# Performance work log

Measured on AMD Instinct MI355X. Metric: run time of the kernel, lower is better.

The kernel has to match this reference:

```python
import jax, jax.numpy as jnp
import numpy as np

HEADS = 8
DIM_HEAD = 96
INNER = HEADS * DIM_HEAD  # 768
PEP_DIM = 768
PRO_DIM = 768
SCALE = DIM_HEAD ** -0.5
NEG = -1000000.0
EPS = 1e-5


def _layer_norm(x, g, b):
    mu = jnp.mean(x, axis=-1, keepdims=True)
    var = jnp.mean(jnp.square(x - mu), axis=-1, keepdims=True)
    return (x - mu) * jax.lax.rsqrt(var + EPS) * g + b


def setup_inputs() -> dict:
    key = jax.random.key(0)
    ks = jax.random.split(key, 12)
    b, n, m = 16, 128, 2048
    peptide = jax.random.normal(ks[0], (b, n, PEP_DIM), dtype=jnp.float32)
    protein = jax.random.normal(ks[1], (b, m, PRO_DIM), dtype=jnp.float32)
    peptide_mask = jax.random.randint(ks[2], (b, n), 0, 2, dtype=jnp.int32)
    pro_mask = jax.random.randint(ks[3], (b, m), 0, 2, dtype=jnp.int32)
    s = 0.02
    Wq = jax.random.normal(ks[4], (PEP_DIM, INNER), dtype=jnp.float32) * s
    Wk = jax.random.normal(ks[5], (PRO_DIM, INNER), dtype=jnp.float32) * s
    Wv_prot = jax.random.normal(ks[6], (PRO_DIM, INNER), dtype=jnp.float32) * s
    Wv_pep = jax.random.normal(ks[7], (PEP_DIM, INNER), dtype=jnp.float32) * s
    Wo_prot = jax.random.normal(ks[8], (INNER, PEP_DIM), dtype=jnp.float32) * s
    bo_prot = jnp.zeros((PEP_DIM,), dtype=jnp.float32)
    Wo_pep = jax.random.normal(ks[9], (INNER, PRO_DIM), dtype=jnp.float32) * s
    bo_pep = jnp.zeros((PRO_DIM,), dtype=jnp.float32)
    ln_g = jnp.ones((PEP_DIM,), dtype=jnp.float32)
    ln_b = jnp.zeros((PEP_DIM,), dtype=jnp.float32)
    return {
        'peptide': peptide, 'protein': protein,
        'peptide_mask': peptide_mask, 'pro_mask': pro_mask,
        'Wq': Wq, 'Wk': Wk, 'Wv_prot': Wv_prot, 'Wv_pep': Wv_pep,
        'Wo_prot': Wo_prot, 'bo_prot': bo_prot,
        'Wo_pep': Wo_pep, 'bo_pep': bo_pep,
        'ln_g': ln_g, 'ln_b': ln_b,
    }


def reference(peptide, protein, peptide_mask, pro_mask,
              Wq, Wk, Wv_prot, Wv_pep, Wo_prot, bo_prot, Wo_pep, bo_pep,
              ln_g, ln_b):
    b, n, _ = peptide.shape
    m = protein.shape[1]
    # projections -> (b, h, len, d)
    q = (peptide @ Wq).reshape(b, n, HEADS, DIM_HEAD).transpose(0, 2, 1, 3)
    k = (protein @ Wk).reshape(b, m, HEADS, DIM_HEAD).transpose(0, 2, 1, 3)
    v_prot = (protein @ Wv_prot).reshape(b, m, HEADS, DIM_HEAD).transpose(0, 2, 1, 3)
    v_pep = (peptide @ Wv_pep).reshape(b, n, HEADS, DIM_HEAD).transpose(0, 2, 1, 3)
    # scores (b, h, n, m)
    dots = jnp.einsum('bhnd,bhmd->bhnm', q, k) * SCALE
    dots = jnp.where(peptide_mask[:, None, :, None] == 0, NEG, dots)
    dots = jnp.where(pro_mask[:, None, None, :] == 0, NEG, dots)
    attn = jax.nn.softmax(dots, axis=-1)
    # peptide-side output: rows of attn aggregate protein values
    out_protein = jnp.einsum('bhnm,bhmd->bhnd', attn, v_prot)
    out_protein = out_protein.transpose(0, 2, 1, 3).reshape(b, n, INNER)
    out_protein = out_protein @ Wo_prot + bo_prot
    out_protein = _layer_norm(out_protein + peptide, ln_g, ln_b)
    # protein-side output: attn^T aggregates peptide values
    out_peptide = jnp.einsum('bhnm,bhnd->bhmd', attn, v_pep)
    out_peptide = out_peptide.transpose(0, 2, 1, 3).reshape(b, m, INNER)
    out_peptide = out_peptide @ Wo_pep + bo_pep
    out_peptide = _layer_norm(out_peptide + protein, ln_g, ln_b)
    return (out_protein, out_peptide, attn)
```

## Files before the change

### kernel.cpp

```cpp
#include <hip/hip_runtime.h>
#include <math.h>

static constexpr int HEADS  = 8;
static constexpr int DHEAD  = 96;
static constexpr int INNER  = 768;
static constexpr int NPEP   = 128;
static constexpr int MPRO   = 2048;
static constexpr float ATT_SCALE = 0.10206207261596577f;
static constexpr float NEGF   = -1000000.0f;
static constexpr float LN_EPS = 1e-5f;

typedef __attribute__((ext_vector_type(8))) short bf16x8;
typedef __attribute__((ext_vector_type(4))) float f32x4;

__device__ __forceinline__ unsigned short f2b(float f) {
    unsigned u = __builtin_bit_cast(unsigned, f);
    u += 0x7fffu + ((u >> 16) & 1u);
    return (unsigned short)(u >> 16);
}
__device__ __forceinline__ float b2f(unsigned short u) {
    return __builtin_bit_cast(float, (unsigned)u << 16);
}

__device__ __forceinline__ void async16(const unsigned short* g, unsigned short* l) {
    __builtin_amdgcn_global_load_lds(
        (const __attribute__((address_space(1))) void*)g,
        (__attribute__((address_space(3))) void*)l, 16, 0, 0);
}

template<int TM, int MODE>
__global__ __launch_bounds__(256) void gemm_bf16(
    const unsigned short* __restrict__ A, const unsigned short* __restrict__ B,
    unsigned short* __restrict__ C,
    int M, int N, int K, int lda, int ldb, int ldc,
    long sAb, long sAh, long sBb, long sBh, long sCb, long sCh,
    const int* __restrict__ mRow, const int* __restrict__ mCol, int lenShift)
{
    constexpr int FR = TM / 32;
    __shared__ unsigned short As[TM * 32];
    __shared__ unsigned short Bs[128 * 32];

    const int tid = threadIdx.x;
    const int n0  = blockIdx.x * 128;
    const int m0  = blockIdx.y * TM;
    const int z   = blockIdx.z;
    const int zb  = z >> 3, zh = z & 7;

    const unsigned short* Ab = A + zb * sAb + zh * sAh;
    const unsigned short* Bb = B + zb * sBb + zh * sBh;

    const int rS = tid >> 2;
    const int kS = (tid & 3) * 8;
    const int wave = tid >> 6;
    unsigned short* ldsA0 = As + wave * 512;
    unsigned short* ldsA1 = As + 2048 + wave * 512;
    unsigned short* ldsB0 = Bs + wave * 512;
    unsigned short* ldsB1 = Bs + 2048 + wave * 512;

    const int lane = tid & 63;
    const int l16  = lane & 15;
    const int quad = lane >> 4;
    const int wr   = (wave >> 1) * (TM / 2);
    const int wc   = (wave & 1) * 64;

    f32x4 acc[FR][4];
#pragma unroll
    for (int i = 0; i < FR; ++i)
#pragma unroll
        for (int j = 0; j < 4; ++j) acc[i][j] = (f32x4){0.f, 0.f, 0.f, 0.f};

    for (int k0 = 0; k0 < K; k0 += 32) {
        async16(Ab + (long)(m0 + rS) * lda + k0 + kS, ldsA0);
        if (TM == 128)
            async16(Ab + (long)(m0 + 64 + rS) * lda + k0 + kS, ldsA1);
        int bR0 = n0 + rS;      if (bR0 > N - 1) bR0 = N - 1;
        int bR1 = n0 + 64 + rS; if (bR1 > N - 1) bR1 = N - 1;
        async16(Bb + (long)bR0 * ldb + k0 + kS, ldsB0);
        async16(Bb + (long)bR1 * ldb + k0 + kS, ldsB1);
        __syncthreads();

        bf16x8 af[FR], bfr[4];
#pragma unroll
        for (int i = 0; i < FR; ++i)
            af[i] = *reinterpret_cast<const bf16x8*>(&As[(wr + i * 16 + l16) * 32 + quad * 8]);
#pragma unroll
        for (int j = 0; j < 4; ++j)
            bfr[j] = *reinterpret_cast<const bf16x8*>(&Bs[(wc + j * 16 + l16) * 32 + quad * 8]);
#pragma unroll
        for (int i = 0; i < FR; ++i)
#pragma unroll
            for (int j = 0; j < 4; ++j)
                acc[i][j] = __builtin_amdgcn_mfma_f32_16x16x32_bf16(af[i], bfr[j], acc[i][j], 0, 0, 0);
        __syncthreads();
    }

#pragma unroll
    for (int i = 0; i < FR; ++i) {
#pragma unroll
        for (int j = 0; j < 4; ++j) {
            const int col = n0 + wc + j * 16 + l16;
            if ((MODE == 2) && col >= N) continue;
            const int h = col / 96, d = col - h * 96;
#pragma unroll
            for (int r = 0; r < 4; ++r) {
                const int row = m0 + wr + i * 16 + quad * 4 + r;
                float v = acc[i][j][r];
                if (MODE == 1) {
                    v *= ATT_SCALE;
                    if (mRow[zb * NPEP + row] == 0 || mCol[zb * MPRO + col] == 0) v = NEGF;
                    C[zb * sCb + zh * sCh + (long)row * ldc + col] = f2b(v);
                } else if (MODE == 2) {
                    C[zb * sCb + zh * sCh + (long)row * ldc + col] = f2b(v);
                } else if (MODE == 3) {
                    const int b = row >> lenShift, rr = row & ((1 << lenShift) - 1);
                    C[(((long)(b * 8 + h) << lenShift) + rr) * 96 + d] = f2b(v);
                } else {
                    const int b = row >> lenShift, rr = row & ((1 << lenShift) - 1);
                    C[(((long)(b * 8 + h) * 96 + d) << lenShift) + rr] = f2b(v);
                }
            }
        }
    }
}

__global__ __launch_bounds__(256) void pv2_kernel(
    const unsigned short* __restrict__ attn16,
    const unsigned short* __restrict__ vpepT,
    unsigned short* __restrict__ opep)
{
    __shared__ unsigned short At[128 * 136];
    __shared__ unsigned short Bv[128 * 136];

    const int tid = threadIdx.x;
    const int m0  = blockIdx.x * 128;
    const int z   = blockIdx.y;
    const int b   = z >> 3, h = z & 7;

    const unsigned short* Az = attn16 + (long)z * NPEP * MPRO;
    const unsigned short* Bz = vpepT + (long)z * 96 * 128;

    {
        const int r = tid >> 1, half = tid & 1;
        const int rc = r > 95 ? 95 : r;
#pragma unroll
        for (int e = 0; e < 8; ++e) {
            bf16x8 v = *reinterpret_cast<const bf16x8*>(Bz + rc * 128 + half * 64 + e * 8);
            *reinterpret_cast<bf16x8*>(&Bv[r * 136 + half * 64 + e * 8]) = v;
        }
    }
    {
        const int mBase = (tid & 7) * 16;
#pragma unroll
        for (int nn = 0; nn < 128; nn += 32) {
            const int n = nn + (tid >> 3);
#pragma unroll
            for (int c = 0; c < 2; ++c) {
                bf16x8 v = *reinterpret_cast<const bf16x8*>(Az + (long)n * MPRO + m0 + mBase + c * 8);
#pragma unroll
                for (int j = 0; j < 8; ++j)
                    At[(mBase + c * 8 + j) * 136 + n] = (unsigned short)v[j];
            }
        }
    }
    __syncthreads();

    const int lane = tid & 63;
    const int l16  = lane & 15;
    const int quad = lane >> 4;
    const int wave = tid >> 6;
    const int wr   = (wave >> 1) * 64;
    const int wc   = (wave & 1) * 64;

    f32x4 acc[4][4];
#pragma unroll
    for (int i = 0; i < 4; ++i)
#pragma unroll
        for (int j = 0; j < 4; ++j) acc[i][j] = (f32x4){0.f, 0.f, 0.f, 0.f};

#pragma unroll
    for (int kc = 0; kc < 4; ++kc) {
        bf16x8 af[4], bfr[4];
#pragma unroll
        for (int i = 0; i < 4; ++i)
            af[i] = *reinterpret_cast<const bf16x8*>(&At[(wr + i * 16 + l16) * 136 + kc * 32 + quad * 8]);
#pragma unroll
        for (int j = 0; j < 4; ++j)
            bfr[j] = *reinterpret_cast<const bf16x8*>(&Bv[(wc + j * 16 + l16) * 136 + kc * 32 + quad * 8]);
#pragma unroll
        for (int i = 0; i < 4; ++i)
#pragma unroll
            for (int j = 0; j < 4; ++j)
                acc[i][j] = __builtin_amdgcn_mfma_f32_16x16x32_bf16(af[i], bfr[j], acc[i][j], 0, 0, 0);
    }

#pragma unroll
    for (int i = 0; i < 4; ++i) {
#pragma unroll
        for (int j = 0; j < 4; ++j) {
            const int d = wc + j * 16 + l16;
            if (d >= 96) continue;
#pragma unroll
            for (int r = 0; r < 4; ++r) {
                const int m = m0 + wr + i * 16 + quad * 4 + r;
                opep[(long)b * MPRO * INNER + (long)m * INNER + h * 96 + d] = f2b(acc[i][j][r]);
            }
        }
    }
}

__global__ __launch_bounds__(256) void conv2_kernel(
    const float* __restrict__ pro, const float* __restrict__ pep,
    unsigned short* __restrict__ pro16, unsigned short* __restrict__ pep16,
    int nPro4, int nPep4)
{
    const int i = blockIdx.x * 256 + threadIdx.x;
    const float* in; unsigned short* out; int idx;
    if (i < nPro4) { in = pro; out = pro16; idx = i; }
    else { idx = i - nPro4; if (idx >= nPep4) return; in = pep; out = pep16; }
    float4 v = reinterpret_cast<const float4*>(in)[idx];
    ushort4 o;
    o.x = f2b(v.x); o.y = f2b(v.y); o.z = f2b(v.z); o.w = f2b(v.w);
    reinterpret_cast<ushort4*>(out)[idx] = o;
}

__global__ __launch_bounds__(256) void wtrans_kernel(
    const float* w0, const float* w1, const float* w2,
    const float* w3, const float* w4, const float* w5,
    unsigned short* o0, unsigned short* o1, unsigned short* o2,
    unsigned short* o3, unsigned short* o4, unsigned short* o5)
{
    const float* in; unsigned short* out;
    switch (blockIdx.z) {
        case 0: in = w0; out = o0; break;
        case 1: in = w1; out = o1; break;
        case 2: in = w2; out = o2; break;
        case 3: in = w3; out = o3; break;
        case 4: in = w4; out = o4; break;
        default: in = w5; out = o5; break;
    }
    __shared__ unsigned short t[32][33];
    const int bx = blockIdx.x * 32, by = blockIdx.y * 32;
    const int x = threadIdx.x, y = threadIdx.y;
#pragma unroll
    for (int i = 0; i < 32; i += 8)
        t[y + i][x] = f2b(in[(long)(by + y + i) * 768 + bx + x]);
    __syncthreads();
#pragma unroll
    for (int i = 0; i < 32; i += 8)
        out[(long)(bx + y + i) * 768 + by + x] = t[x][y + i];
}

__global__ __launch_bounds__(256) void softmax_kernel(
    unsigned short* __restrict__ s16, float* __restrict__ attn)
{
    __shared__ float smx[4], sms[4];
    const long row = blockIdx.x;
    unsigned short* p16 = s16 + row * (long)MPRO;
    float* pf = attn + row * (long)MPRO;
    const int tid = threadIdx.x;
    const int wv = tid >> 6;

    float v[8];
    float mx = -3.4e38f;
#pragma unroll
    for (int k = 0; k < 8; ++k) { v[k] = b2f(p16[tid + k * 256]); mx = fmaxf(mx, v[k]); }
#pragma unroll
    for (int off = 32; off > 0; off >>= 1) mx = fmaxf(mx, __shfl_xor(mx, off));
    if ((tid & 63) == 0) smx[wv] = mx;
    __syncthreads();
    mx = fmaxf(fmaxf(smx[0], smx[1]), fmaxf(smx[2], smx[3]));

    float sum = 0.f;
#pragma unroll
    for (int k = 0; k < 8; ++k) { v[k] = __expf(v[k] - mx); sum += v[k]; }
#pragma unroll
    for (int off = 32; off > 0; off >>= 1) sum += __shfl_xor(sum, off);
    if ((tid & 63) == 0) sms[wv] = sum;
    __syncthreads();
    const float inv = 1.0f / (sms[0] + sms[1] + sms[2] + sms[3]);
#pragma unroll
    for (int k = 0; k < 8; ++k) {
        const float o = v[k] * inv;
        pf[tid + k * 256] = o;
        p16[tid + k * 256] = f2b(o);
    }
}

__global__ __launch_bounds__(256) void bias_res_ln(
    const unsigned short* __restrict__ tmp, const float* __restrict__ bias,
    const float* __restrict__ res, const float* __restrict__ gam,
    const float* __restrict__ bet, float* __restrict__ out)
{
    __shared__ float red[8];
    const long row = blockIdx.x;
    const unsigned short* t = tmp + row * INNER;
    const float* r = res + row * INNER;
    float* o = out + row * INNER;
    const int tid = threadIdx.x;
    const int wv = tid >> 6;

    float v[3]; float s = 0.f;
#pragma unroll
    for (int k = 0; k < 3; ++k) { const int c = tid + k * 256; v[k] = b2f(t[c]) + bias[c] + r[c]; s += v[k]; }
#pragma unroll
    for (int off = 32; off > 0; off >>= 1) s += __shfl_xor(s, off);
    if ((tid & 63) == 0) red[wv] = s;
    __syncthreads();
    const float mu = (red[0] + red[1] + red[2] + red[3]) * (1.0f / INNER);

    float vs = 0.f;
#pragma unroll
    for (int k = 0; k < 3; ++k) { const float d = v[k] - mu; vs += d * d; }
#pragma unroll
    for (int off = 32; off > 0; off >>= 1) vs += __shfl_xor(vs, off);
    if ((tid & 63) == 0) red[4 + wv] = vs;
    __syncthreads();
    const float rstd = rsqrtf((red[4] + red[5] + red[6] + red[7]) * (1.0f / INNER) + LN_EPS);
#pragma unroll
    for (int k = 0; k < 3; ++k) { const int c = tid + k * 256; o[c] = (v[k] - mu) * rstd * gam[c] + bet[c]; }
}

extern "C" void kernel_launch(void* const* d_in, const int* in_sizes, int n_in,
                              void* d_out, int out_size, void* d_ws, size_t ws_size,
                              hipStream_t stream)
{
    (void)in_sizes; (void)n_in; (void)out_size; (void)ws_size;

    const float* peptide = (const float*)d_in[0];
    const float* protein = (const float*)d_in[1];
    const int*   pepm    = (const int*)  d_in[2];
    const int*   prom    = (const int*)  d_in[3];
    const float* Wq      = (const float*)d_in[4];
    const float* Wk      = (const float*)d_in[5];
    const float* Wv_prot = (const float*)d_in[6];
    const float* Wv_pep  = (const float*)d_in[7];
    const float* Wo_prot = (const float*)d_in[8];
    const float* bo_prot = (const float*)d_in[9];
    const float* Wo_pep  = (const float*)d_in[10];
    const float* bo_pep  = (const float*)d_in[11];
    const float* ln_g    = (const float*)d_in[12];
    const float* ln_b    = (const float*)d_in[13];

    char* ws = (char*)d_ws;
    auto U = [&](size_t off) { return (unsigned short*)(ws + off); };
    unsigned short* WT0   = U(0);
    unsigned short* WT1   = U(1179648);
    unsigned short* WT2   = U(2 * 1179648);
    unsigned short* WT3   = U(3 * 1179648);
    unsigned short* WT4   = U(4 * 1179648);
    unsigned short* WT5   = U(5 * 1179648);
    unsigned short* q16   = U(7077888);
    unsigned short* k16   = U(10223616);
    unsigned short* vpT   = U(60555264);
    unsigned short* vpepT = U(110886912);
    unsigned short* s16   = U(114032640);
    unsigned short* pro16 = U(114032640);
    unsigned short* pep16 = U(164364288);
    unsigned short* opp   = U(7077888);
    unsigned short* tmp1  = U(10223616);
    unsigned short* opep  = U(13369344);
    unsigned short* tmp2  = U(63700992);

    float* outP = (float*)d_out;
    float* outQ = outP + 16 * 128 * 768;
    float* attn = outQ + (long)16 * 2048 * 768;

    conv2_kernel<<<26112, 256, 0, stream>>>(protein, peptide, pro16, pep16, 6291456, 393216);
    wtrans_kernel<<<dim3(24, 24, 6), dim3(32, 8), 0, stream>>>(
        Wq, Wk, Wv_prot, Wv_pep, Wo_prot, Wo_pep, WT0, WT1, WT2, WT3, WT4, WT5);

    gemm_bf16<128, 3><<<dim3(6, 16, 1), 256, 0, stream>>>(
        pep16, WT0, q16, 2048, 768, 768, 768, 768, 0,
        0, 0, 0, 0, 0, 0, nullptr, nullptr, 7);
    gemm_bf16<128, 3><<<dim3(6, 256, 1), 256, 0, stream>>>(
        pro16, WT1, k16, 32768, 768, 768, 768, 768, 0,
        0, 0, 0, 0, 0, 0, nullptr, nullptr, 11);
    gemm_bf16<128, 4><<<dim3(6, 256, 1), 256, 0, stream>>>(
        pro16, WT2, vpT, 32768, 768, 768, 768, 768, 0,
        0, 0, 0, 0, 0, 0, nullptr, nullptr, 11);
    gemm_bf16<128, 4><<<dim3(6, 16, 1), 256, 0, stream>>>(
        pep16, WT3, vpepT, 2048, 768, 768, 768, 768, 0,
        0, 0, 0, 0, 0, 0, nullptr, nullptr, 7);

    gemm_bf16<128, 1><<<dim3(16, 1, 128), 256, 0, stream>>>(
        q16, k16, s16, 128, 2048, 96, 96, 96, 2048,
        98304L, 12288L, 1572864L, 196608L, 2097152L, 262144L, pepm, prom, 0);

    softmax_kernel<<<16384, 256, 0, stream>>>(s16, attn);

    gemm_bf16<64, 2><<<dim3(1, 2, 128), 256, 0, stream>>>(
        s16, vpT, opp, 128, 96, 2048, 2048, 2048, 768,
        2097152L, 262144L, 1572864L, 196608L, 98304L, 96L, nullptr, nullptr, 0);

    gemm_bf16<64, 2><<<dim3(6, 32, 1), 256, 0, stream>>>(
        opp, WT4, tmp1, 2048, 768, 768, 768, 768, 768,
        0, 0, 0, 0, 0, 0, nullptr, nullptr, 0);
    bias_res_ln<<<2048, 256, 0, stream>>>(tmp1, bo_prot, peptide, ln_g, ln_b, outP);

    pv2_kernel<<<dim3(16, 128), 256, 0, stream>>>(s16, vpepT, opep);

    gemm_bf16<128, 2><<<dim3(6, 256, 1), 256, 0, stream>>>(
        opep, WT5, tmp2, 32768, 768, 768, 768, 768, 768,
        0, 0, 0, 0, 0, 0, nullptr, nullptr, 0);
    bias_res_ln<<<32768, 256, 0, stream>>>(tmp2, bo_pep, protein, ln_g, ln_b, outQ);
}
```

Before: 831.3 us.

## Triple-buffer GEMM LDS loads, swizzle large-GEMM blocks, move masking into softmax

The bf16 GEMM now keeps three LDS stages of async global-to-LDS loads in flight. It waits on explicit vmcnt counts and raw barriers instead of a sync per k-step, and raises wave priority around the MFMA block. The large protein-side GEMMs use a flattened 1D grid with an XCD-aware block swizzle to improve L2 locality. Score masking moves out of the QK GEMM epilogue into the softmax kernel, which reads the peptide and protein masks itself. The extra LDS stages use more shared memory and may lower occupancy, and the hand-written waitcnt values depend on the exact number of async loads issued per stage.

```diff
diff --git a/kernel.cpp b/kernel.cpp
--- a/kernel.cpp
+++ b/kernel.cpp
@@ -34,15 +34,25 @@
     unsigned short* __restrict__ C,
     int M, int N, int K, int lda, int ldb, int ldc,
     long sAb, long sAh, long sBb, long sBh, long sCb, long sCh,
-    const int* __restrict__ mRow, const int* __restrict__ mCol, int lenShift)
-{
-    constexpr int FR = TM / 32;
-    __shared__ unsigned short As[TM * 32];
-    __shared__ unsigned short Bs[128 * 32];
+    const int* __restrict__ mRow, const int* __restrict__ mCol, int lenShift,
+    int nxSwz)
+{
+    (void)mRow; (void)mCol; (void)M;
+    constexpr int FR   = TM / 32;
+    constexpr int PIPE = 3;
+    __shared__ unsigned short As[PIPE][TM * 32];
+    __shared__ unsigned short Bs[PIPE][128 * 32];
 
     const int tid = threadIdx.x;
-    const int n0  = blockIdx.x * 128;
-    const int m0  = blockIdx.y * TM;
+    int bx, by;
+    if (nxSwz > 0) {
+        const int bid = blockIdx.x;
+        const int per = gridDim.x >> 3;
+        const int v   = (bid & 7) * per + (bid >> 3);
+        bx = v % nxSwz; by = v / nxSwz;
+    } else { bx = blockIdx.x; by = blockIdx.y; }
+    const int n0  = bx * 128;
+    const int m0  = by * TM;
     const int z   = blockIdx.z;
     const int zb  = z >> 3, zh = z & 7;
 
@@ -52,10 +62,6 @@
     const int rS = tid >> 2;
     const int kS = (tid & 3) * 8;
     const int wave = tid >> 6;
-    unsigned short* ldsA0 = As + wave * 512;
-    unsigned short* ldsA1 = As + 2048 + wave * 512;
-    unsigned short* ldsB0 = Bs + wave * 512;
-    unsigned short* ldsB1 = Bs + 2048 + wave * 512;
 
     const int lane = tid & 63;
     const int l16  = lane & 15;
@@ -69,29 +75,58 @@
 #pragma unroll
         for (int j = 0; j < 4; ++j) acc[i][j] = (f32x4){0.f, 0.f, 0.f, 0.f};
 
-    for (int k0 = 0; k0 < K; k0 += 32) {
-        async16(Ab + (long)(m0 + rS) * lda + k0 + kS, ldsA0);
+    auto stageT = [&](int t, int bi) {
+        const int k0 = t << 5;
+        unsigned short* a0 = &As[bi][wave * 512];
+        async16(Ab + (long)(m0 + rS) * lda + k0 + kS, a0);
         if (TM == 128)
-            async16(Ab + (long)(m0 + 64 + rS) * lda + k0 + kS, ldsA1);
+            async16(Ab + (long)(m0 + 64 + rS) * lda + k0 + kS, a0 + 2048);
         int bR0 = n0 + rS;      if (bR0 > N - 1) bR0 = N - 1;
         int bR1 = n0 + 64 + rS; if (bR1 > N - 1) bR1 = N - 1;
-        async16(Bb + (long)bR0 * ldb + k0 + kS, ldsB0);
-        async16(Bb + (long)bR1 * ldb + k0 + kS, ldsB1);
-        __syncthreads();
+        unsigned short* b0 = &Bs[bi][wave * 512];
+        async16(Bb + (long)bR0 * ldb + k0 + kS, b0);
+        async16(Bb + (long)bR1 * ldb + k0 + kS, b0 + 2048);
+    };
+
+    const int NT = K >> 5;
+    stageT(0, 0);
+    if (NT > 1) stageT(1, 1);
+    if (NT > 2) stageT(2, 2);
+
+    int bi = 0;
+    for (int t = 0; t < NT; ++t) {
+        const int ahead = NT - 1 - t;
+        if constexpr (TM == 128) {
+            if (ahead >= 2)      asm volatile("s_waitcnt vmcnt(8)" ::: "memory");
+            else if (ahead == 1) asm volatile("s_waitcnt vmcnt(4)" ::: "memory");
+            else                 asm volatile("s_waitcnt vmcnt(0)" ::: "memory");
+        } else {
+            if (ahead >= 2)      asm volatile("s_waitcnt vmcnt(6)" ::: "memory");
+            else if (ahead == 1) asm volatile("s_waitcnt vmcnt(3)" ::: "memory");
+            else                 asm volatile("s_waitcnt vmcnt(0)" ::: "memory");
+        }
+        __builtin_amdgcn_s_barrier();
 
         bf16x8 af[FR], bfr[4];
 #pragma unroll
         for (int i = 0; i < FR; ++i)
-            af[i] = *reinterpret_cast<const bf16x8*>(&As[(wr + i * 16 + l16) * 32 + quad * 8]);
+            af[i] = *reinterpret_cast<const bf16x8*>(&As[bi][(wr + i * 16 + l16) * 32 + quad * 8]);
 #pragma unroll
         for (int j = 0; j < 4; ++j)
-            bfr[j] = *reinterpret_cast<const bf16x8*>(&Bs[(wc + j * 16 + l16) * 32 + quad * 8]);
+            bfr[j] = *reinterpret_cast<const bf16x8*>(&Bs[bi][(wc + j * 16 + l16) * 32 + quad * 8]);
+
+        __builtin_amdgcn_s_setprio(1);
 #pragma unroll
         for (int i = 0; i < FR; ++i)
 #pragma unroll
             for (int j = 0; j < 4; ++j)
                 acc[i][j] = __builtin_amdgcn_mfma_f32_16x16x32_bf16(af[i], bfr[j], acc[i][j], 0, 0, 0);
-        __syncthreads();
+        __builtin_amdgcn_s_setprio(0);
+
+        __builtin_amdgcn_s_barrier();
+        __builtin_amdgcn_sched_barrier(0);
+        if (t + PIPE < NT) stageT(t + PIPE, bi);
+        bi = bi + 1; if (bi == PIPE) bi = 0;
     }
 
 #pragma unroll
@@ -107,7 +142,6 @@
                 float v = acc[i][j][r];
                 if (MODE == 1) {
                     v *= ATT_SCALE;
-                    if (mRow[zb * NPEP + row] == 0 || mCol[zb * MPRO + col] == 0) v = NEGF;
                     C[zb * sCb + zh * sCh + (long)row * ldc + col] = f2b(v);
                 } else if (MODE == 2) {
                     C[zb * sCb + zh * sCh + (long)row * ldc + col] = f2b(v);
@@ -251,19 +285,34 @@
 }
 
 __global__ __launch_bounds__(256) void softmax_kernel(
-    unsigned short* __restrict__ s16, float* __restrict__ attn)
+    unsigned short* __restrict__ s16, float* __restrict__ attn,
+    const int* __restrict__ pepm, const int* __restrict__ prom)
 {
     __shared__ float smx[4], sms[4];
     const long row = blockIdx.x;
+    const int b = (int)(row >> 10);
+    const int n = (int)(row & 127);
     unsigned short* p16 = s16 + row * (long)MPRO;
     float* pf = attn + row * (long)MPRO;
     const int tid = threadIdx.x;
     const int wv = tid >> 6;
+    const int rowOk = pepm[(b << 7) + n];
 
     float v[8];
     float mx = -3.4e38f;
-#pragma unroll
-    for (int k = 0; k < 8; ++k) { v[k] = b2f(p16[tid + k * 256]); mx = fmaxf(mx, v[k]); }
+    if (rowOk) {
+#pragma unroll
+        for (int k = 0; k < 8; ++k) {
+            const int c = tid + k * 256;
+            float x = b2f(p16[c]);
+            if (prom[(b << 11) + c] == 0) x = NEGF;
+            v[k] = x; mx = fmaxf(mx, x);
+        }
+    } else {
+#pragma unroll
+        for (int k = 0; k < 8; ++k) v[k] = NEGF;
+        mx = NEGF;
+    }
 #pragma unroll
     for (int off = 32; off > 0; off >>= 1) mx = fmaxf(mx, __shfl_xor(mx, off));
     if ((tid & 63) == 0) smx[wv] = mx;
@@ -371,36 +420,36 @@
 
     gemm_bf16<128, 3><<<dim3(6, 16, 1), 256, 0, stream>>>(
         pep16, WT0, q16, 2048, 768, 768, 768, 768, 0,
-        0, 0, 0, 0, 0, 0, nullptr, nullptr, 7);
-    gemm_bf16<128, 3><<<dim3(6, 256, 1), 256, 0, stream>>>(
+        0, 0, 0, 0, 0, 0, nullptr, nullptr, 7, 0);
+    gemm_bf16<128, 3><<<dim3(1536, 1, 1), 256, 0, stream>>>(
         pro16, WT1, k16, 32768, 768, 768, 768, 768, 0,
-        0, 0, 0, 0, 0, 0, nullptr, nullptr, 11);
-    gemm_bf16<128, 4><<<dim3(6, 256, 1), 256, 0, stream>>>(
+        0, 0, 0, 0, 0, 0, nullptr, nullptr, 11, 6);
+    gemm_bf16<128, 4><<<dim3(1536, 1, 1), 256, 0, stream>>>(
         pro16, WT2, vpT, 32768, 768, 768, 768, 768, 0,
-        0, 0, 0, 0, 0, 0, nullptr, nullptr, 11);
+        0, 0, 0, 0, 0, 0, nullptr, nullptr, 11, 6);
     gemm_bf16<128, 4><<<dim3(6, 16, 1), 256, 0, stream>>>(
         pep16, WT3, vpepT, 2048, 768, 768, 768, 768, 0,
-        0, 0, 0, 0, 0, 0, nullptr, nullptr, 7);
+        0, 0, 0, 0, 0, 0, nullptr, nullptr, 7, 0);
 
     gemm_bf16<128, 1><<<dim3(16, 1, 128), 256, 0, stream>>>(
         q16, k16, s16, 128, 2048, 96, 96, 96, 2048,
-        98304L, 12288L, 1572864L, 196608L, 2097152L, 262144L, pepm, prom, 0);
-
-    softmax_kernel<<<16384, 256, 0, stream>>>(s16, attn);
+        98304L, 12288L, 1572864L, 196608L, 2097152L, 262144L, nullptr, nullptr, 0, 0);
+
+    softmax_kernel<<<16384, 256, 0, stream>>>(s16, attn, pepm, prom);
 
     gemm_bf16<64, 2><<<dim3(1, 2, 128), 256, 0, stream>>>(
         s16, vpT, opp, 128, 96, 2048, 2048, 2048, 768,
-        2097152L, 262144L, 1572864L, 196608L, 98304L, 96L, nullptr, nullptr, 0);
+        2097152L, 262144L, 1572864L, 196608L, 98304L, 96L, nullptr, nullptr, 0, 0);
 
     gemm_bf16<64, 2><<<dim3(6, 32, 1), 256, 0, stream>>>(
         opp, WT4, tmp1, 2048, 768, 768, 768, 768, 768,
-        0, 0, 0, 0, 0, 0, nullptr, nullptr, 0);
+        0, 0, 0, 0, 0, 0, nullptr, nullptr, 0, 0);
     bias_res_ln<<<2048, 256, 0, stream>>>(tmp1, bo_prot, peptide, ln_g, ln_b, outP);
 
     pv2_kernel<<<dim3(16, 128), 256, 0, stream>>>(s16, vpepT, opep);
 
-    gemm_bf16<128, 2><<<dim3(6, 256, 1), 256, 0, stream>>>(
+    gemm_bf16<128, 2><<<dim3(1536, 1, 1), 256, 0, stream>>>(
         opep, WT5, tmp2, 32768, 768, 768, 768, 768, 768,
-        0, 0, 0, 0, 0, 0, nullptr, nullptr, 0);
+        0, 0, 0, 0, 0, 0, nullptr, nullptr, 0, 6);
     bias_res_ln<<<32768, 256, 0, stream>>>(tmp2, bo_pep, protein, ln_g, ln_b, outQ);
 }
```

Measured after the change: 754.1 us. -9.3%, faster.
